# Kernel tuning notes

Measured on AMD Instinct MI355X. Metric: run time of the kernel, lower is better.

Reference implementation:

```python
import jax, jax.numpy as jnp
import numpy as np

B, N, U, D = 64, 1024, 128, 2   # batch, num_nodes, num_units, output_dim
K, L = 2, 2                     # max_diffusion_step, num_layers
NM = 2 * K + 1                  # num_matrices: 2 supports (dual random walk) * K + identity


def setup_inputs():
    key = jax.random.key(0)
    ks = jax.random.split(key, 16)
    d0, d1 = D + U, U + U       # gconv input_size per layer
    s = 0.05
    return {
        "inputs": jax.random.normal(ks[0], (B, N * D), jnp.float32),
        "hidden_state": jax.random.normal(ks[1], (L, B, N * U), jnp.float32),
        "adj": jax.random.uniform(ks[2], (N, N), dtype=jnp.float32),
        "gate_w0": jax.random.normal(ks[3], (d0 * NM, 2 * U), jnp.float32) * s,
        "gate_b0": jnp.ones((2 * U,), jnp.float32),   # bias_start=1.0 as in DCGRU gate
        "cand_w0": jax.random.normal(ks[4], (d0 * NM, U), jnp.float32) * s,
        "cand_b0": jnp.zeros((U,), jnp.float32),
        "gate_w1": jax.random.normal(ks[5], (d1 * NM, 2 * U), jnp.float32) * s,
        "gate_b1": jnp.ones((2 * U,), jnp.float32),
        "cand_w1": jax.random.normal(ks[6], (d1 * NM, U), jnp.float32) * s,
        "cand_b1": jnp.zeros((U,), jnp.float32),
        "proj_w": jax.random.normal(ks[7], (U, D), jnp.float32) * s,
        "proj_b": jnp.zeros((D,), jnp.float32),
    }


def _supports(adj):
    # dual random walk: [ (D_o^-1 A)^T, (D_i^-1 A^T)^T ]
    rw = lambda a: a / jnp.sum(a, axis=1, keepdims=True)
    return [rw(adj).T, rw(adj.T).T]


def _gconv(supports, x_bnd, h_bnd, w, b):
    # x_bnd: (B,N,in_dim), h_bnd: (B,N,U)
    in_size = x_bnd.shape[-1] + U
    x0 = jnp.transpose(jnp.concatenate([x_bnd, h_bnd], axis=-1), (1, 2, 0)).reshape(N, in_size * B)
    xs = [x0]
    for S in supports:
        xk_2, xk_1 = x0, S @ x0
        xs.append(xk_1)
        for _ in range(2, K + 1):
            xk = 2.0 * (S @ xk_1) - xk_2   # Chebyshev recursion
            xs.append(xk)
            xk_2, xk_1 = xk_1, xk
    x = jnp.stack(xs)                                   # (NM, N, in_size*B)
    x = x.reshape(NM, N, in_size, B).transpose(3, 1, 2, 0).reshape(B * N, in_size * NM)
    return x @ w + b                                    # (B*N, out)


def _dcgru_cell(supports, x_flat, h_flat, gw, gb, cw, cb, in_dim):
    xb = x_flat.reshape(B, N, in_dim)
    hb = h_flat.reshape(B, N, U)
    ru = jax.nn.sigmoid(_gconv(supports, xb, hb, gw, gb)).reshape(B, N, 2 * U)
    r, u = ru[..., :U], ru[..., U:]
    c = jnp.tanh(_gconv(supports, xb, r * hb, cw, cb)).reshape(B, N, U)
    return (u * hb + (1.0 - u) * c).reshape(B, N * U)


def reference(inputs, hidden_state, adj, gate_w0, gate_b0, cand_w0, cand_b0,
              gate_w1, gate_b1, cand_w1, cand_b1, proj_w, proj_b):
    sup = _supports(adj)
    h0 = _dcgru_cell(sup, inputs, hidden_state[0], gate_w0, gate_b0, cand_w0, cand_b0, D)
    h1 = _dcgru_cell(sup, h0, hidden_state[1], gate_w1, gate_b1, cand_w1, cand_b1, U)
    out = (h1.reshape(B * N, U) @ proj_w + proj_b).reshape(B, N * D)
    return out, jnp.stack([h0, h1])
```

## Files before the change

### kernel.cpp

```cpp
#include <hip/hip_runtime.h>
#include <hip/hip_bf16.h>

typedef unsigned short u16;
typedef unsigned int u32;
typedef __attribute__((ext_vector_type(2))) unsigned int u32x2;
typedef __attribute__((ext_vector_type(4))) float f32x4;
typedef __attribute__((ext_vector_type(8))) __bf16 bf16x8;

#define DEVI static __device__ __forceinline__

DEVI u16 f2bf(float x) {
  union { float f; u32 u; } v; v.f = x;
  u32 r = v.u + 0x7fffu + ((v.u >> 16) & 1u);
  return (u16)(r >> 16);
}
DEVI float bf2f(u16 h) { union { u32 u; float f; } v; v.u = ((u32)h) << 16; return v.f; }
DEVI u32 pk2bf(float a, float b) { return (u32)f2bf(a) | ((u32)f2bf(b) << 16); }
DEVI float sigm(float x) { return 1.f / (1.f + __expf(-x)); }
DEVI float tanh_(float x) {
  float a = fabsf(x);
  float e = __expf(-2.f * a);
  float t = (1.f - e) / (1.f + e);
  return copysignf(t, x);
}

DEVI void gl_lds16(const u16* g, void* l) {
  __builtin_amdgcn_global_load_lds(
      (const __attribute__((address_space(1))) u32*)(const void*)g,
      (__attribute__((address_space(3))) u32*)l, 16, 0, 0);
}
DEVI f32x4 mfma16(bf16x8 a, bf16x8 b, f32x4 c) {
  return __builtin_amdgcn_mfma_f32_16x16x32_bf16(a, b, c, 0, 0, 0);
}

#define SWZ(row) (((row) >> 1) & 3)

__global__ void sums_k(const float* __restrict__ adj, float* __restrict__ rs, float* __restrict__ cs) {
  __shared__ float red[256];
  int bid = blockIdx.x, tid = threadIdx.x;
  if (bid < 1024) {
    float a = 0.f;
    for (int j = tid; j < 1024; j += 256) a += adj[bid * 1024 + j];
    red[tid] = a; __syncthreads();
    for (int s = 128; s; s >>= 1) { if (tid < s) red[tid] += red[tid + s]; __syncthreads(); }
    if (!tid) rs[bid] = red[0];
  } else {
    int c0 = (bid - 1024) * 64;
    int c = tid & 63, r0 = tid >> 6;
    float a = 0.f;
    for (int r = r0; r < 1024; r += 4) a += adj[r * 1024 + c0 + c];
    red[tid] = a; __syncthreads();
    if (tid < 64) cs[c0 + c] = red[c] + red[64 + c] + red[128 + c] + red[192 + c];
  }
}

__global__ void s0_build(const float* __restrict__ adj, const float* __restrict__ rs, u16* __restrict__ S0) {
  __shared__ float tile[32][33];
  int i0 = blockIdx.x * 32, j0 = blockIdx.y * 32;
  int tx = threadIdx.x & 31, ty = threadIdx.x >> 5;
  for (int yy = ty; yy < 32; yy += 8)
    tile[yy][tx] = adj[(j0 + yy) * 1024 + i0 + tx];
  __syncthreads();
  for (int yy = ty; yy < 32; yy += 8)
    S0[(i0 + yy) * 1024 + j0 + tx] = f2bf(tile[tx][yy] / rs[j0 + tx]);
}

__global__ void s1_build(const float* __restrict__ adj, const float* __restrict__ cs, u16* __restrict__ S1) {
  int idx = blockIdx.x * 256 + threadIdx.x;
  int j = idx & 1023;
  S1[idx] = f2bf(adj[idx] / cs[j]);
}

__global__ void pack_w(const float* __restrict__ src, u16* __restrict__ dst,
                       int NO, int Ktot, int off0, int off1) {
  int idx = blockIdx.x * 256 + threadIdx.x;
  if (idx >= NO * Ktot) return;
  int o = idx / Ktot, k = idx % Ktot;
  int seg = k >> 7, i = k & 127;
  int mo = seg % 6;
  int pos = ((seg / 6) ? off1 : off0) + i;
  const float* wr = src + (long)pos * 5 * NO + o;
  float v;
  switch (mo) {
    case 0: case 1: v = wr[0] - wr[(long)2 * NO] - wr[(long)4 * NO]; break;
    case 2: v = wr[(long)1 * NO]; break;
    case 3: v = 2.f * wr[(long)2 * NO]; break;
    case 4: v = wr[(long)3 * NO]; break;
    default: v = 2.f * wr[(long)4 * NO]; break;
  }
  dst[idx] = f2bf(v);
}

__global__ void build_hx(const float* __restrict__ src, u16* __restrict__ hiN,
                         u16* __restrict__ loN, u16* __restrict__ hiT) {
  __shared__ u16 t[32][33];
  int n0 = blockIdx.x * 32, u0 = blockIdx.y * 32, b = blockIdx.z;
  int tx = threadIdx.x & 31, ty = threadIdx.x >> 5;
  for (int yy = ty; yy < 32; yy += 8) {
    long d = (long)b * 131072 + (n0 + yy) * 128 + u0 + tx;
    float v = src[d];
    u16 h = f2bf(v);
    hiN[d] = h;
    loN[d] = f2bf(v - bf2f(h));
    t[yy][tx] = h;
  }
  __syncthreads();
  for (int yy = ty; yy < 32; yy += 8)
    hiT[(long)(b * 128 + u0 + yy) * 1024 + n0 + tx] = t[tx][yy];
}

__global__ void xch0_build(const float* __restrict__ inp, float* __restrict__ x0) {
  int idx = blockIdx.x * 256 + threadIdx.x;
  int n = idx >> 7, c = idx & 127, b = c >> 1, d = c & 1;
  x0[idx] = inp[b * 2048 + n * 2 + d];
}

__global__ void xch_diffuse(const u16* __restrict__ S, const float* __restrict__ xin,
                            float* __restrict__ xout) {
  int n = blockIdx.x, c = threadIdx.x;
  float acc = 0.f;
  for (int k = 0; k < 1024; k++) acc += bf2f(S[n * 1024 + k]) * xin[k * 128 + c];
  xout[n * 128 + c] = acc;
}

__global__ void xch_cheb(const u16* __restrict__ S, const float* __restrict__ xin,
                         const float* __restrict__ x0, float* __restrict__ xout) {
  int n = blockIdx.x, c = threadIdx.x;
  float acc = 0.f;
  for (int k = 0; k < 1024; k++) acc += bf2f(S[n * 1024 + k]) * xin[k * 128 + c];
  xout[n * 128 + c] = 2.f * acc - x0[n * 128 + c];
}

__global__ void xg_build(const float* __restrict__ gw0, const float* __restrict__ cw0,
                         const float* __restrict__ xch,
                         u16* __restrict__ xgg, u16* __restrict__ xgc) {
  int r = blockIdx.x;
  int n = r & 1023, b = r >> 10;
  int t = threadIdx.x;
  __shared__ float xv[10];
  if (t < 10) { int m = t % 5, p = t / 5; xv[t] = xch[(long)m * 131072 + n * 128 + b * 2 + p]; }
  __syncthreads();
  float a = 0.f;
#pragma unroll
  for (int q = 0; q < 10; q++) { int m = q % 5, p = q / 5;
    a += gw0[(long)(p * 5 + m) * 256 + t] * xv[q]; }
  xgg[(long)r * 256 + t] = f2bf(a);
  if (t < 128) {
    float a2 = 0.f;
#pragma unroll
    for (int q = 0; q < 10; q++) { int m = q % 5, p = q / 5;
      a2 += cw0[(long)(p * 5 + m) * 128 + t] * xv[q]; }
    xgc[(long)r * 128 + t] = f2bf(a2);
  }
}

struct DiffJob { const u16* X; const u16* S; u16* YN; u16* YT; };
struct DiffJobs { DiffJob j[4]; };

__global__ __launch_bounds__(256, 2) void gemm_diffz(DiffJobs jobs) {
  DiffJob J = jobs.j[blockIdx.z];
  constexpr int ROWS = 384;
  constexpr int BUF = ROWS * 64;
  __shared__ char smem[3 * BUF];
  const int tid = threadIdx.x, wid = tid >> 6, lane = tid & 63;
  const int wrM = wid >> 1, wcN = wid & 1, l15 = lane & 15, l4 = lane >> 4;
  const int s_row = lane >> 2, s_kcp = lane & 3;
  const int ntile = blockIdx.y * 256;
  const int fbase = blockIdx.x * 128;

  f32x4 acc[8][4];
#pragma unroll
  for (int i = 0; i < 8; i++)
#pragma unroll
    for (int j = 0; j < 4; j++) acc[i][j] = (f32x4){0.f, 0.f, 0.f, 0.f};

  auto stage = [&](char* buf, int ks) {
    const int k0 = ks * 32;
#pragma unroll
    for (int c = 0; c < 6; c++) {
      const int row0 = c * 64 + wid * 16;
      const int row = row0 + s_row;
      const u16* src;
      if (row0 < 256) src = J.S + (long)(ntile + row) * 1024 + k0 + ((s_kcp ^ SWZ(row)) * 8);
      else { const int fr = row - 256; src = J.X + (long)(fbase + fr) * 1024 + k0 + ((s_kcp ^ SWZ(fr)) * 8); }
      gl_lds16(src, buf + row0 * 64);
    }
  };
  auto compute = [&](char* buf) {
    char* Ab = buf; char* Bb = buf + 256 * 64;
    bf16x8 af[8], bfr[4];
#pragma unroll
    for (int mb = 0; mb < 8; mb++) {
      const int row = wrM * 128 + mb * 16 + l15;
      af[mb] = *(const bf16x8*)(Ab + row * 64 + ((l4 ^ SWZ(row)) * 16));
    }
#pragma unroll
    for (int nb = 0; nb < 4; nb++) {
      const int row = wcN * 64 + nb * 16 + l15;
      bfr[nb] = *(const bf16x8*)(Bb + row * 64 + ((l4 ^ SWZ(row)) * 16));
    }
    __builtin_amdgcn_s_setprio(1);
#pragma unroll
    for (int mb = 0; mb < 8; mb++)
#pragma unroll
      for (int nb = 0; nb < 4; nb++)
        acc[mb][nb] = mfma16(af[mb], bfr[nb], acc[mb][nb]);
    __builtin_amdgcn_s_setprio(0);
  };

  const int NKS = 32;
  stage(smem, 0);
  stage(smem + BUF, 1);
  char* cur = smem; char* mid = smem + BUF; char* fut = smem + 2 * BUF;
  for (int ks = 0; ks + 2 < NKS; ks++) {
    stage(fut, ks + 2);
    asm volatile("s_waitcnt vmcnt(12)" ::: "memory");
    __builtin_amdgcn_s_barrier();
    __builtin_amdgcn_sched_barrier(0);
    compute(cur);
    asm volatile("" ::: "memory");
    __builtin_amdgcn_s_barrier();
    __builtin_amdgcn_sched_barrier(0);
    char* t = cur; cur = mid; mid = fut; fut = t;
  }
  asm volatile("s_waitcnt vmcnt(6)" ::: "memory");
  __builtin_amdgcn_s_barrier();
  __builtin_amdgcn_sched_barrier(0);
  compute(cur);
  asm volatile("s_waitcnt vmcnt(0)" ::: "memory");
  __builtin_amdgcn_s_barrier();
  __builtin_amdgcn_sched_barrier(0);
  compute(mid);

#pragma unroll
  for (int mb = 0; mb < 8; mb++) {
#pragma unroll
    for (int nb = 0; nb < 4; nb++) {
      const int n0 = ntile + wrM * 128 + mb * 16 + l4 * 4;
      const int f  = fbase + wcN * 64 + nb * 16 + l15;
      const int b = f >> 7, u = f & 127;
      f32x4 v = acc[mb][nb];
      u16 h0 = f2bf(v[0]), h1 = f2bf(v[1]), h2 = f2bf(v[2]), h3 = f2bf(v[3]);
      u16* yn = J.YN + (long)b * 131072 + (long)n0 * 128 + u;
      yn[0] = h0; yn[128] = h1; yn[256] = h2; yn[384] = h3;
      if (J.YT != nullptr) {
        u32x2 wv; wv[0] = (u32)h0 | ((u32)h1 << 16); wv[1] = (u32)h2 | ((u32)h3 << 16);
        *(u32x2*)(J.YT + (long)f * 1024 + n0) = wv;
      }
    }
  }
}

struct Segs { const u16* p[12]; };
DEVI const u16* seg_sel(const Segs& s, int i) {
  switch (i) {
    case 0: return s.p[0]; case 1: return s.p[1]; case 2: return s.p[2];
    case 3: return s.p[3]; case 4: return s.p[4]; case 5: return s.p[5];
    case 6: return s.p[6]; case 7: return s.p[7]; case 8: return s.p[8];
    case 9: return s.p[9]; case 10: return s.p[10]; default: return s.p[11];
  }
}

template<int EPI>
__global__ __launch_bounds__(256, 2) void gemm_wseg(
    Segs segs, const u16* __restrict__ WT, int Ktot,
    const float* __restrict__ bias, const float* __restrict__ Hprev,
    const u16* __restrict__ xadd,
    u16* __restrict__ rh_hi, u16* __restrict__ rh_lo, u16* __restrict__ rh_t,
    u16* __restrict__ usig,
    float* __restrict__ hnew_out, u16* __restrict__ xa_hi, u16* __restrict__ xa_lo,
    u16* __restrict__ xa_t)
{
  constexpr int TM = (EPI == 0) ? 256 : 128;
  constexpr int MB = (EPI == 0) ? 8 : 4;
  constexpr int MW = (EPI == 0) ? 128 : 64;
  constexpr int R1 = (TM + 128) / 64;
  constexpr int BUF = (TM + 128) * 64;
  __shared__ char smem[3 * BUF];
  const int tid = threadIdx.x, wid = tid >> 6, lane = tid & 63;
  const int wrM = wid >> 1, wcN = wid & 1, l15 = lane & 15, l4 = lane >> 4;
  const int s_row = lane >> 2, s_kcp = lane & 3;
  const int rtile = blockIdx.x * 128;

  f32x4 acc[MB][4];
#pragma unroll
  for (int i = 0; i < MB; i++)
#pragma unroll
    for (int j = 0; j < 4; j++) acc[i][j] = (f32x4){0.f, 0.f, 0.f, 0.f};

  const int NKS = Ktot >> 5;
  auto stage = [&](char* buf, int ks) {
    const int k0 = ks * 32;
    const int sidx = ks >> 2, si0 = (ks & 3) * 32;
    const u16* sp = seg_sel(segs, sidx);
#pragma unroll
    for (int c = 0; c < R1; c++) {
      const int row0 = c * 64 + wid * 16;
      const int row = row0 + s_row;
      const u16* src;
      if (row0 < TM) src = WT + (long)row * Ktot + k0 + ((s_kcp ^ SWZ(row)) * 8);
      else { const int br = row - TM; src = sp + (long)(rtile + br) * 128 + si0 + ((s_kcp ^ SWZ(br)) * 8); }
      gl_lds16(src, buf + row0 * 64);
    }
  };
  auto compute = [&](char* buf) {
    char* Ab = buf; char* Bb = buf + TM * 64;
    bf16x8 af[MB], bfr[4];
#pragma unroll
    for (int mb = 0; mb < MB; mb++) {
      const int row = wrM * MW + mb * 16 + l15;
      af[mb] = *(const bf16x8*)(Ab + row * 64 + ((l4 ^ SWZ(row)) * 16));
    }
#pragma unroll
    for (int nb = 0; nb < 4; nb++) {
      const int row = wcN * 64 + nb * 16 + l15;
      bfr[nb] = *(const bf16x8*)(Bb + row * 64 + ((l4 ^ SWZ(row)) * 16));
    }
    __builtin_amdgcn_s_setprio(1);
#pragma unroll
    for (int mb = 0; mb < MB; mb++)
#pragma unroll
      for (int nb = 0; nb < 4; nb++)
        acc[mb][nb] = mfma16(af[mb], bfr[nb], acc[mb][nb]);
    __builtin_amdgcn_s_setprio(0);
  };

  stage(smem, 0);
  stage(smem + BUF, 1);
  char* cur = smem; char* mid = smem + BUF; char* fut = smem + 2 * BUF;
  for (int ks = 0; ks + 2 < NKS; ks++) {
    stage(fut, ks + 2);
    if constexpr (R1 == 6) asm volatile("s_waitcnt vmcnt(12)" ::: "memory");
    else                   asm volatile("s_waitcnt vmcnt(8)" ::: "memory");
    __builtin_amdgcn_s_barrier();
    __builtin_amdgcn_sched_barrier(0);
    compute(cur);
    asm volatile("" ::: "memory");
    __builtin_amdgcn_s_barrier();
    __builtin_amdgcn_sched_barrier(0);
    char* t = cur; cur = mid; mid = fut; fut = t;
  }
  if constexpr (R1 == 6) asm volatile("s_waitcnt vmcnt(6)" ::: "memory");
  else                   asm volatile("s_waitcnt vmcnt(4)" ::: "memory");
  __builtin_amdgcn_s_barrier();
  __builtin_amdgcn_sched_barrier(0);
  compute(cur);
  asm volatile("s_waitcnt vmcnt(0)" ::: "memory");
  __builtin_amdgcn_s_barrier();
  __builtin_amdgcn_sched_barrier(0);
  compute(mid);

#pragma unroll
  for (int mb = 0; mb < MB; mb++) {
#pragma unroll
    for (int nb = 0; nb < 4; nb++) {
      const int o = wrM * MW + mb * 16 + l4 * 4;
      const int rr = rtile + wcN * 64 + nb * 16 + l15;
      const int n = rr & 1023, b = rr >> 10;
      f32x4 v = acc[mb][nb];
      float4 bv = *(const float4*)(bias + o);
      float a0 = 0.f, a1 = 0.f, a2 = 0.f, a3 = 0.f;
      if (xadd != nullptr) {
        const int xs = (EPI == 0) ? 256 : 128;
        u32x2 xv = *(const u32x2*)(xadd + (long)rr * xs + o);
        a0 = bf2f((u16)(xv[0] & 0xffffu)); a1 = bf2f((u16)(xv[0] >> 16));
        a2 = bf2f((u16)(xv[1] & 0xffffu)); a3 = bf2f((u16)(xv[1] >> 16));
      }
      if (EPI == 0) {
        float s0 = sigm(v[0] + bv.x + a0), s1 = sigm(v[1] + bv.y + a1);
        float s2 = sigm(v[2] + bv.z + a2), s3 = sigm(v[3] + bv.w + a3);
        if (o < 128) {
          float4 hv = *(const float4*)(Hprev + (long)rr * 128 + o);
          float r0 = s0 * hv.x, r1 = s1 * hv.y, r2 = s2 * hv.z, r3 = s3 * hv.w;
          u16 h0 = f2bf(r0), h1 = f2bf(r1), h2 = f2bf(r2), h3 = f2bf(r3);
          long d = (long)rr * 128 + o;
          u32x2 wh; wh[0] = (u32)h0 | ((u32)h1 << 16); wh[1] = (u32)h2 | ((u32)h3 << 16);
          *(u32x2*)(rh_hi + d) = wh;
          u32x2 wl; wl[0] = pk2bf(r0 - bf2f(h0), r1 - bf2f(h1));
          wl[1] = pk2bf(r2 - bf2f(h2), r3 - bf2f(h3));
          *(u32x2*)(rh_lo + d) = wl;
          u16* rt = rh_t + (long)(b * 128 + o) * 1024 + n;
          rt[0] = h0; rt[1024] = h1; rt[2048] = h2; rt[3072] = h3;
        } else {
          u32x2 wu; wu[0] = pk2bf(s0, s1); wu[1] = pk2bf(s2, s3);
          *(u32x2*)(usig + (long)rr * 128 + (o - 128)) = wu;
        }
      } else {
        float c0 = tanh_(v[0] + bv.x + a0), c1 = tanh_(v[1] + bv.y + a1);
        float c2 = tanh_(v[2] + bv.z + a2), c3 = tanh_(v[3] + bv.w + a3);
        u32x2 uv = *(const u32x2*)(usig + (long)rr * 128 + o);
        float u0 = bf2f((u16)(uv[0] & 0xffffu)), u1 = bf2f((u16)(uv[0] >> 16));
        float u2 = bf2f((u16)(uv[1] & 0xffffu)), u3 = bf2f((u16)(uv[1] >> 16));
        float4 hv = *(const float4*)(Hprev + (long)rr * 128 + o);
        float h0n = u0 * hv.x + (1.f - u0) * c0;
        float h1n = u1 * hv.y + (1.f - u1) * c1;
        float h2n = u2 * hv.z + (1.f - u2) * c2;
        float h3n = u3 * hv.w + (1.f - u3) * c3;
        *(float4*)(hnew_out + (long)rr * 128 + o) = make_float4(h0n, h1n, h2n, h3n);
        if (xa_hi != nullptr) {
          u16 x0 = f2bf(h0n), x1 = f2bf(h1n), x2 = f2bf(h2n), x3 = f2bf(h3n);
          long d = (long)rr * 128 + o;
          u32x2 wh; wh[0] = (u32)x0 | ((u32)x1 << 16); wh[1] = (u32)x2 | ((u32)x3 << 16);
          *(u32x2*)(xa_hi + d) = wh;
          u32x2 wl; wl[0] = pk2bf(h0n - bf2f(x0), h1n - bf2f(x1));
          wl[1] = pk2bf(h2n - bf2f(x2), h3n - bf2f(x3));
          *(u32x2*)(xa_lo + d) = wl;
          u16* xt = xa_t + (long)(b * 128 + o) * 1024 + n;
          xt[0] = x0; xt[1024] = x1; xt[2048] = x2; xt[3072] = x3;
        }
      }
    }
  }
}

__global__ __launch_bounds__(256) void proj_k(const float* __restrict__ h1n, const float* __restrict__ pw,
                                              const float* __restrict__ pb, float* __restrict__ out) {
  int wid = threadIdx.x >> 6, lane = threadIdx.x & 63;
  int r = blockIdx.x * 4 + wid;
  int b = r >> 10, n = r & 1023;
  const float* hp = h1n + (long)b * 131072 + n * 128;
  float ha = hp[lane], hb = hp[lane + 64];
  float p0 = ha * pw[lane * 2]     + hb * pw[(lane + 64) * 2];
  float p1 = ha * pw[lane * 2 + 1] + hb * pw[(lane + 64) * 2 + 1];
  for (int off = 32; off; off >>= 1) { p0 += __shfl_down(p0, off); p1 += __shfl_down(p1, off); }
  if (!lane) {
    out[(long)b * 2048 + n * 2]     = p0 + pb[0];
    out[(long)b * 2048 + n * 2 + 1] = p1 + pb[1];
  }
}

extern "C" void kernel_launch(void* const* d_in, const int* in_sizes, int n_in,
                              void* d_out, int out_size, void* d_ws, size_t ws_size,
                              hipStream_t stream) {
  (void)in_sizes; (void)n_in; (void)out_size; (void)ws_size;
  const float* inputs = (const float*)d_in[0];
  const float* hidden = (const float*)d_in[1];
  const float* adj    = (const float*)d_in[2];
  const float* gw0 = (const float*)d_in[3];
  const float* gb0 = (const float*)d_in[4];
  const float* cw0 = (const float*)d_in[5];
  const float* cb0 = (const float*)d_in[6];
  const float* gw1 = (const float*)d_in[7];
  const float* gb1 = (const float*)d_in[8];
  const float* cw1 = (const float*)d_in[9];
  const float* cb1 = (const float*)d_in[10];
  const float* pw  = (const float*)d_in[11];
  const float* pb  = (const float*)d_in[12];

  float* out    = (float*)d_out;
  float* out_h0 = out + 131072;
  float* out_h1 = out_h0 + 8388608;
  const float* h0 = hidden;
  const float* h1 = hidden + 8388608;

  u16* OH1a = (u16*)out_h1;
  u16* OH1b = OH1a + 8388608;

  char* wp = (char*)d_ws;
  auto alloc = [&](size_t bytes) { char* r = wp; wp += (bytes + 255) & ~(size_t)255; return r; };
  u16*   S0b  = (u16*)  alloc(1048576 * 2);
  u16*   S1b  = (u16*)  alloc(1048576 * 2);
  float* rs   = (float*)alloc(1024 * 4);
  float* cs   = (float*)alloc(1024 * 4);
  u16*   WG0  = (u16*)  alloc((size_t)256 * 768 * 2);
  u16*   WC0  = (u16*)  alloc((size_t)128 * 768 * 2);
  u16*   WG1  = (u16*)  alloc((size_t)256 * 1536 * 2);
  u16*   WC1  = (u16*)  alloc((size_t)128 * 1536 * 2);
  u16*   Bb   = (u16*)  alloc((size_t)13 * 8388608 * 2);
  u16*   USIG = (u16*)  alloc((size_t)8388608 * 2);
  float* XCH  = (float*)alloc((size_t)5 * 131072 * 4);
  auto BB = [&](int i) { return Bb + (size_t)i * 8388608; };
  auto XC = [&](int i) { return XCH + (size_t)i * 131072; };
  u16* XGg = BB(4);
  u16* XGc = BB(6);

  sums_k<<<1040, 256, 0, stream>>>(adj, rs, cs);
  s0_build<<<dim3(32, 32), 256, 0, stream>>>(adj, rs, S0b);
  s1_build<<<4096, 256, 0, stream>>>(adj, cs, S1b);
  pack_w<<<768,  256, 0, stream>>>(gw0, WG0, 256, 768, 2, 0);
  pack_w<<<384,  256, 0, stream>>>(cw0, WC0, 128, 768, 2, 0);
  pack_w<<<1536, 256, 0, stream>>>(gw1, WG1, 256, 1536, 0, 128);
  pack_w<<<768,  256, 0, stream>>>(cw1, WC1, 128, 1536, 0, 128);
  build_hx<<<dim3(32, 4, 64), 256, 0, stream>>>(h0, BB(0), BB(1), BB(2));
  build_hx<<<dim3(32, 4, 64), 256, 0, stream>>>(h1, OH1a, OH1b, BB(3));

  xch0_build<<<512, 256, 0, stream>>>(inputs, XC(0));
  xch_diffuse<<<1024, 128, 0, stream>>>(S0b, XC(0), XC(1));
  xch_cheb   <<<1024, 128, 0, stream>>>(S0b, XC(1), XC(0), XC(2));
  xch_diffuse<<<1024, 128, 0, stream>>>(S1b, XC(0), XC(3));
  xch_cheb   <<<1024, 128, 0, stream>>>(S1b, XC(3), XC(0), XC(4));
  xg_build<<<65536, 256, 0, stream>>>(gw0, cw0, XCH, XGg, XGc);

  DiffJobs dj{};
  dj.j[0] = {BB(2), S0b, BB(7), BB(8)};
  dj.j[1] = {BB(2), S1b, BB(9), BB(10)};
  gemm_diffz<<<dim3(64, 4, 2), 256, 0, stream>>>(dj);
  dj.j[0] = {BB(8),  S0b, BB(11), nullptr};
  dj.j[1] = {BB(10), S1b, BB(12), nullptr};
  gemm_diffz<<<dim3(64, 4, 2), 256, 0, stream>>>(dj);

  Segs sg0{};
  sg0.p[0] = BB(0); sg0.p[1] = BB(1); sg0.p[2] = BB(7); sg0.p[3] = BB(11); sg0.p[4] = BB(9); sg0.p[5] = BB(12);
  gemm_wseg<0><<<512, 256, 0, stream>>>(sg0, WG0, 768, gb0, h0, XGg,
      BB(2), BB(10), BB(8), USIG, nullptr, nullptr, nullptr, nullptr);

  dj.j[0] = {BB(8), S0b, BB(4), BB(5)};
  dj.j[1] = {BB(8), S1b, BB(0), BB(1)};
  gemm_diffz<<<dim3(64, 4, 2), 256, 0, stream>>>(dj);
  dj.j[0] = {BB(5), S0b, BB(7), nullptr};
  dj.j[1] = {BB(1), S1b, BB(9), nullptr};
  gemm_diffz<<<dim3(64, 4, 2), 256, 0, stream>>>(dj);

  Segs sc0{};
  sc0.p[0] = BB(2); sc0.p[1] = BB(10); sc0.p[2] = BB(4); sc0.p[3] = BB(7); sc0.p[4] = BB(0); sc0.p[5] = BB(9);
  gemm_wseg<1><<<512, 256, 0, stream>>>(sc0, WC0, 768, cb0, h0, XGc,
      nullptr, nullptr, nullptr, USIG, out_h0, BB(11), BB(12), BB(1));

  dj.j[0] = {BB(1), S0b, BB(0), BB(2)};
  dj.j[1] = {BB(1), S1b, BB(4), BB(5)};
  dj.j[2] = {BB(3), S0b, BB(8), BB(6)};
  dj.j[3] = {BB(3), S1b, BB(9), BB(7)};
  gemm_diffz<<<dim3(64, 4, 4), 256, 0, stream>>>(dj);
  dj.j[0] = {BB(2), S0b, BB(10), nullptr};
  dj.j[1] = {BB(5), S1b, BB(3),  nullptr};
  gemm_diffz<<<dim3(64, 4, 2), 256, 0, stream>>>(dj);
  dj.j[0] = {BB(6), S0b, BB(1), nullptr};
  dj.j[1] = {BB(7), S1b, BB(2), nullptr};
  gemm_diffz<<<dim3(64, 4, 2), 256, 0, stream>>>(dj);

  Segs sg1{};
  sg1.p[0] = BB(11); sg1.p[1] = BB(12); sg1.p[2] = BB(0); sg1.p[3] = BB(10); sg1.p[4] = BB(4); sg1.p[5] = BB(3);
  sg1.p[6] = OH1a;   sg1.p[7] = OH1b;   sg1.p[8] = BB(8); sg1.p[9] = BB(1);  sg1.p[10] = BB(9); sg1.p[11] = BB(2);
  gemm_wseg<0><<<512, 256, 0, stream>>>(sg1, WG1, 1536, gb1, h1, nullptr,
      BB(5), BB(7), BB(6), USIG, nullptr, nullptr, nullptr, nullptr);

  dj.j[0] = {BB(6), S0b, BB(8), BB(1)};
  dj.j[1] = {BB(6), S1b, BB(9), BB(2)};
  gemm_diffz<<<dim3(64, 4, 2), 256, 0, stream>>>(dj);
  dj.j[0] = {BB(1), S0b, BB(6), nullptr};
  gemm_diffz<<<dim3(64, 4, 1), 256, 0, stream>>>(dj);
  dj.j[0] = {BB(2), S1b, BB(1), nullptr};
  gemm_diffz<<<dim3(64, 4, 1), 256, 0, stream>>>(dj);

  Segs sc1{};
  sc1.p[0] = BB(11); sc1.p[1] = BB(12); sc1.p[2] = BB(0); sc1.p[3] = BB(10); sc1.p[4] = BB(4); sc1.p[5] = BB(3);
  sc1.p[6] = BB(5);  sc1.p[7] = BB(7);  sc1.p[8] = BB(8); sc1.p[9] = BB(6);  sc1.p[10] = BB(9); sc1.p[11] = BB(1);
  gemm_wseg<1><<<512, 256, 0, stream>>>(sc1, WC1, 1536, cb1, h1, nullptr,
      nullptr, nullptr, nullptr, USIG, out_h1, nullptr, nullptr, nullptr);

  proj_k<<<16384, 256, 0, stream>>>(out_h1, pw, pb, out);
}
```

Measured before the change: 1.115 ms.

## Drop bf16 hi/lo split of identity term and batch xg_build rows per block

Removes the low-residual bf16 copy of the hidden and intermediate states that the projection GEMMs used as an extra K-segment for the identity term. This shrinks the weight K from 6 to 5 segments per input and removes the lo writes in build_hx and both GEMM epilogues. Buffers are reassigned to match. Separately, xg_build now caches its weights in shared memory and processes 32 rows per block instead of one row per block. The cost is lower precision on the identity term of the graph convolution.

```diff
diff --git a/kernel.cpp b/kernel.cpp
--- a/kernel.cpp
+++ b/kernel.cpp
@@ -77,31 +77,29 @@
   if (idx >= NO * Ktot) return;
   int o = idx / Ktot, k = idx % Ktot;
   int seg = k >> 7, i = k & 127;
-  int mo = seg % 6;
-  int pos = ((seg / 6) ? off1 : off0) + i;
+  int mo = seg % 5;
+  int pos = ((seg / 5) ? off1 : off0) + i;
   const float* wr = src + (long)pos * 5 * NO + o;
   float v;
   switch (mo) {
-    case 0: case 1: v = wr[0] - wr[(long)2 * NO] - wr[(long)4 * NO]; break;
-    case 2: v = wr[(long)1 * NO]; break;
-    case 3: v = 2.f * wr[(long)2 * NO]; break;
-    case 4: v = wr[(long)3 * NO]; break;
+    case 0: v = wr[0] - wr[(long)2 * NO] - wr[(long)4 * NO]; break;
+    case 1: v = wr[(long)1 * NO]; break;
+    case 2: v = 2.f * wr[(long)2 * NO]; break;
+    case 3: v = wr[(long)3 * NO]; break;
     default: v = 2.f * wr[(long)4 * NO]; break;
   }
   dst[idx] = f2bf(v);
 }
 
 __global__ void build_hx(const float* __restrict__ src, u16* __restrict__ hiN,
-                         u16* __restrict__ loN, u16* __restrict__ hiT) {
+                         u16* __restrict__ hiT) {
   __shared__ u16 t[32][33];
   int n0 = blockIdx.x * 32, u0 = blockIdx.y * 32, b = blockIdx.z;
   int tx = threadIdx.x & 31, ty = threadIdx.x >> 5;
   for (int yy = ty; yy < 32; yy += 8) {
     long d = (long)b * 131072 + (n0 + yy) * 128 + u0 + tx;
-    float v = src[d];
-    u16 h = f2bf(v);
+    u16 h = f2bf(src[d]);
     hiN[d] = h;
-    loN[d] = f2bf(v - bf2f(h));
     t[yy][tx] = h;
   }
   __syncthreads();
@@ -131,26 +129,37 @@
   xout[n * 128 + c] = 2.f * acc - x0[n * 128 + c];
 }
 
-__global__ void xg_build(const float* __restrict__ gw0, const float* __restrict__ cw0,
-                         const float* __restrict__ xch,
-                         u16* __restrict__ xgg, u16* __restrict__ xgc) {
-  int r = blockIdx.x;
-  int n = r & 1023, b = r >> 10;
+__global__ __launch_bounds__(256) void xg_build(
+    const float* __restrict__ gw0, const float* __restrict__ cw0,
+    const float* __restrict__ xch,
+    u16* __restrict__ xgg, u16* __restrict__ xgc) {
+  __shared__ float wg[10][256];
+  __shared__ float wc[10][128];
+  __shared__ float xv[10];
   int t = threadIdx.x;
-  __shared__ float xv[10];
-  if (t < 10) { int m = t % 5, p = t / 5; xv[t] = xch[(long)m * 131072 + n * 128 + b * 2 + p]; }
+#pragma unroll
+  for (int q = 0; q < 10; q++) {
+    int m = q % 5, p = q / 5;
+    wg[q][t] = gw0[(long)(p * 5 + m) * 256 + t];
+    if (t < 128) wc[q][t] = cw0[(long)(p * 5 + m) * 128 + t];
+  }
   __syncthreads();
-  float a = 0.f;
-#pragma unroll
-  for (int q = 0; q < 10; q++) { int m = q % 5, p = q / 5;
-    a += gw0[(long)(p * 5 + m) * 256 + t] * xv[q]; }
-  xgg[(long)r * 256 + t] = f2bf(a);
-  if (t < 128) {
-    float a2 = 0.f;
-#pragma unroll
-    for (int q = 0; q < 10; q++) { int m = q % 5, p = q / 5;
-      a2 += cw0[(long)(p * 5 + m) * 128 + t] * xv[q]; }
-    xgc[(long)r * 128 + t] = f2bf(a2);
+  int r0 = blockIdx.x * 32;
+  for (int rl = 0; rl < 32; rl++) {
+    int r = r0 + rl, n = r & 1023, b = r >> 10;
+    if (t < 10) { int m = t % 5, p = t / 5; xv[t] = xch[(long)m * 131072 + n * 128 + b * 2 + p]; }
+    __syncthreads();
+    float a = 0.f;
+#pragma unroll
+    for (int q = 0; q < 10; q++) a += wg[q][t] * xv[q];
+    xgg[(long)r * 256 + t] = f2bf(a);
+    if (t < 128) {
+      float a2 = 0.f;
+#pragma unroll
+      for (int q = 0; q < 10; q++) a2 += wc[q][t] * xv[q];
+      xgc[(long)r * 128 + t] = f2bf(a2);
+    }
+    __syncthreads();
   }
 }
 
@@ -159,8 +168,7 @@
 
 __global__ __launch_bounds__(256, 2) void gemm_diffz(DiffJobs jobs) {
   DiffJob J = jobs.j[blockIdx.z];
-  constexpr int ROWS = 384;
-  constexpr int BUF = ROWS * 64;
+  constexpr int BUF = 384 * 64;
   __shared__ char smem[3 * BUF];
   const int tid = threadIdx.x, wid = tid >> 6, lane = tid & 63;
   const int wrM = wid >> 1, wcN = wid & 1, l15 = lane & 15, l4 = lane >> 4;
@@ -251,13 +259,13 @@
   }
 }
 
-struct Segs { const u16* p[12]; };
+struct Segs { const u16* p[10]; };
 DEVI const u16* seg_sel(const Segs& s, int i) {
   switch (i) {
     case 0: return s.p[0]; case 1: return s.p[1]; case 2: return s.p[2];
     case 3: return s.p[3]; case 4: return s.p[4]; case 5: return s.p[5];
     case 6: return s.p[6]; case 7: return s.p[7]; case 8: return s.p[8];
-    case 9: return s.p[9]; case 10: return s.p[10]; default: return s.p[11];
+    default: return s.p[9];
   }
 }
 
@@ -266,10 +274,8 @@
     Segs segs, const u16* __restrict__ WT, int Ktot,
     const float* __restrict__ bias, const float* __restrict__ Hprev,
     const u16* __restrict__ xadd,
-    u16* __restrict__ rh_hi, u16* __restrict__ rh_lo, u16* __restrict__ rh_t,
-    u16* __restrict__ usig,
-    float* __restrict__ hnew_out, u16* __restrict__ xa_hi, u16* __restrict__ xa_lo,
-    u16* __restrict__ xa_t)
+    u16* __restrict__ rh_hi, u16* __restrict__ rh_t, u16* __restrict__ usig,
+    float* __restrict__ hnew_out, u16* __restrict__ xa_hi, u16* __restrict__ xa_t)
 {
   constexpr int TM = (EPI == 0) ? 256 : 128;
   constexpr int MB = (EPI == 0) ? 8 : 4;
@@ -376,9 +382,6 @@
           long d = (long)rr * 128 + o;
           u32x2 wh; wh[0] = (u32)h0 | ((u32)h1 << 16); wh[1] = (u32)h2 | ((u32)h3 << 16);
           *(u32x2*)(rh_hi + d) = wh;
-          u32x2 wl; wl[0] = pk2bf(r0 - bf2f(h0), r1 - bf2f(h1));
-          wl[1] = pk2bf(r2 - bf2f(h2), r3 - bf2f(h3));
-          *(u32x2*)(rh_lo + d) = wl;
           u16* rt = rh_t + (long)(b * 128 + o) * 1024 + n;
           rt[0] = h0; rt[1024] = h1; rt[2048] = h2; rt[3072] = h3;
         } else {
@@ -402,9 +405,6 @@
           long d = (long)rr * 128 + o;
           u32x2 wh; wh[0] = (u32)x0 | ((u32)x1 << 16); wh[1] = (u32)x2 | ((u32)x3 << 16);
           *(u32x2*)(xa_hi + d) = wh;
-          u32x2 wl; wl[0] = pk2bf(h0n - bf2f(x0), h1n - bf2f(x1));
-          wl[1] = pk2bf(h2n - bf2f(x2), h3n - bf2f(x3));
-          *(u32x2*)(xa_lo + d) = wl;
           u16* xt = xa_t + (long)(b * 128 + o) * 1024 + n;
           xt[0] = x0; xt[1024] = x1; xt[2048] = x2; xt[3072] = x3;
         }
@@ -454,7 +454,6 @@
   const float* h1 = hidden + 8388608;
 
   u16* OH1a = (u16*)out_h1;
-  u16* OH1b = OH1a + 8388608;
 
   char* wp = (char*)d_ws;
   auto alloc = [&](size_t bytes) { char* r = wp; wp += (bytes + 255) & ~(size_t)255; return r; };
@@ -462,91 +461,90 @@
   u16*   S1b  = (u16*)  alloc(1048576 * 2);
   float* rs   = (float*)alloc(1024 * 4);
   float* cs   = (float*)alloc(1024 * 4);
-  u16*   WG0  = (u16*)  alloc((size_t)256 * 768 * 2);
-  u16*   WC0  = (u16*)  alloc((size_t)128 * 768 * 2);
-  u16*   WG1  = (u16*)  alloc((size_t)256 * 1536 * 2);
-  u16*   WC1  = (u16*)  alloc((size_t)128 * 1536 * 2);
+  u16*   WG0  = (u16*)  alloc((size_t)256 * 640 * 2);
+  u16*   WC0  = (u16*)  alloc((size_t)128 * 640 * 2);
+  u16*   WG1  = (u16*)  alloc((size_t)256 * 1280 * 2);
+  u16*   WC1  = (u16*)  alloc((size_t)128 * 1280 * 2);
   u16*   Bb   = (u16*)  alloc((size_t)13 * 8388608 * 2);
   u16*   USIG = (u16*)  alloc((size_t)8388608 * 2);
   float* XCH  = (float*)alloc((size_t)5 * 131072 * 4);
   auto BB = [&](int i) { return Bb + (size_t)i * 8388608; };
   auto XC = [&](int i) { return XCH + (size_t)i * 131072; };
-  u16* XGg = BB(4);
-  u16* XGc = BB(6);
+  u16* XGg = BB(3);
+  u16* XGc = BB(5);
 
   sums_k<<<1040, 256, 0, stream>>>(adj, rs, cs);
   s0_build<<<dim3(32, 32), 256, 0, stream>>>(adj, rs, S0b);
   s1_build<<<4096, 256, 0, stream>>>(adj, cs, S1b);
-  pack_w<<<768,  256, 0, stream>>>(gw0, WG0, 256, 768, 2, 0);
-  pack_w<<<384,  256, 0, stream>>>(cw0, WC0, 128, 768, 2, 0);
-  pack_w<<<1536, 256, 0, stream>>>(gw1, WG1, 256, 1536, 0, 128);
-  pack_w<<<768,  256, 0, stream>>>(cw1, WC1, 128, 1536, 0, 128);
-  build_hx<<<dim3(32, 4, 64), 256, 0, stream>>>(h0, BB(0), BB(1), BB(2));
-  build_hx<<<dim3(32, 4, 64), 256, 0, stream>>>(h1, OH1a, OH1b, BB(3));
+  pack_w<<<640,  256, 0, stream>>>(gw0, WG0, 256, 640, 2, 0);
+  pack_w<<<320,  256, 0, stream>>>(cw0, WC0, 128, 640, 2, 0);
+  pack_w<<<1280, 256, 0, stream>>>(gw1, WG1, 256, 1280, 0, 128);
+  pack_w<<<640,  256, 0, stream>>>(cw1, WC1, 128, 1280, 0, 128);
+  build_hx<<<dim3(32, 4, 64), 256, 0, stream>>>(h0, BB(0), BB(1));
+  build_hx<<<dim3(32, 4, 64), 256, 0, stream>>>(h1, OH1a, BB(2));
 
   xch0_build<<<512, 256, 0, stream>>>(inputs, XC(0));
   xch_diffuse<<<1024, 128, 0, stream>>>(S0b, XC(0), XC(1));
   xch_cheb   <<<1024, 128, 0, stream>>>(S0b, XC(1), XC(0), XC(2));
   xch_diffuse<<<1024, 128, 0, stream>>>(S1b, XC(0), XC(3));
   xch_cheb   <<<1024, 128, 0, stream>>>(S1b, XC(3), XC(0), XC(4));
-  xg_build<<<65536, 256, 0, stream>>>(gw0, cw0, XCH, XGg, XGc);
+  xg_build<<<2048, 256, 0, stream>>>(gw0, cw0, XCH, XGg, XGc);
 
   DiffJobs dj{};
-  dj.j[0] = {BB(2), S0b, BB(7), BB(8)};
-  dj.j[1] = {BB(2), S1b, BB(9), BB(10)};
-  gemm_diffz<<<dim3(64, 4, 2), 256, 0, stream>>>(dj);
-  dj.j[0] = {BB(8),  S0b, BB(11), nullptr};
-  dj.j[1] = {BB(10), S1b, BB(12), nullptr};
+  dj.j[0] = {BB(1), S0b, BB(6), BB(7)};
+  dj.j[1] = {BB(1), S1b, BB(8), BB(9)};
+  gemm_diffz<<<dim3(64, 4, 2), 256, 0, stream>>>(dj);
+  dj.j[0] = {BB(7), S0b, BB(10), nullptr};
+  dj.j[1] = {BB(9), S1b, BB(11), nullptr};
   gemm_diffz<<<dim3(64, 4, 2), 256, 0, stream>>>(dj);
 
   Segs sg0{};
-  sg0.p[0] = BB(0); sg0.p[1] = BB(1); sg0.p[2] = BB(7); sg0.p[3] = BB(11); sg0.p[4] = BB(9); sg0.p[5] = BB(12);
-  gemm_wseg<0><<<512, 256, 0, stream>>>(sg0, WG0, 768, gb0, h0, XGg,
-      BB(2), BB(10), BB(8), USIG, nullptr, nullptr, nullptr, nullptr);
-
-  dj.j[0] = {BB(8), S0b, BB(4), BB(5)};
-  dj.j[1] = {BB(8), S1b, BB(0), BB(1)};
-  gemm_diffz<<<dim3(64, 4, 2), 256, 0, stream>>>(dj);
-  dj.j[0] = {BB(5), S0b, BB(7), nullptr};
-  dj.j[1] = {BB(1), S1b, BB(9), nullptr};
+  sg0.p[0] = BB(0); sg0.p[1] = BB(6); sg0.p[2] = BB(10); sg0.p[3] = BB(8); sg0.p[4] = BB(11);
+  gemm_wseg<0><<<512, 256, 0, stream>>>(sg0, WG0, 640, gb0, h0, XGg,
+      BB(12), BB(1), USIG, nullptr, nullptr, nullptr);
+
+  dj.j[0] = {BB(1), S0b, BB(6), BB(7)};
+  dj.j[1] = {BB(1), S1b, BB(8), BB(9)};
+  gemm_diffz<<<dim3(64, 4, 2), 256, 0, stream>>>(dj);
+  dj.j[0] = {BB(7), S0b, BB(10), nullptr};
+  dj.j[1] = {BB(9), S1b, BB(11), nullptr};
   gemm_diffz<<<dim3(64, 4, 2), 256, 0, stream>>>(dj);
 
   Segs sc0{};
-  sc0.p[0] = BB(2); sc0.p[1] = BB(10); sc0.p[2] = BB(4); sc0.p[3] = BB(7); sc0.p[4] = BB(0); sc0.p[5] = BB(9);
-  gemm_wseg<1><<<512, 256, 0, stream>>>(sc0, WC0, 768, cb0, h0, XGc,
-      nullptr, nullptr, nullptr, USIG, out_h0, BB(11), BB(12), BB(1));
-
-  dj.j[0] = {BB(1), S0b, BB(0), BB(2)};
-  dj.j[1] = {BB(1), S1b, BB(4), BB(5)};
-  dj.j[2] = {BB(3), S0b, BB(8), BB(6)};
-  dj.j[3] = {BB(3), S1b, BB(9), BB(7)};
+  sc0.p[0] = BB(12); sc0.p[1] = BB(6); sc0.p[2] = BB(10); sc0.p[3] = BB(8); sc0.p[4] = BB(11);
+  gemm_wseg<1><<<512, 256, 0, stream>>>(sc0, WC0, 640, cb0, h0, XGc,
+      nullptr, nullptr, USIG, out_h0, BB(0), BB(1));
+
+  dj.j[0] = {BB(1), S0b, BB(3), BB(4)};
+  dj.j[1] = {BB(1), S1b, BB(5), BB(6)};
+  dj.j[2] = {BB(2), S0b, BB(7), BB(8)};
+  dj.j[3] = {BB(2), S1b, BB(9), BB(10)};
   gemm_diffz<<<dim3(64, 4, 4), 256, 0, stream>>>(dj);
-  dj.j[0] = {BB(2), S0b, BB(10), nullptr};
-  dj.j[1] = {BB(5), S1b, BB(3),  nullptr};
-  gemm_diffz<<<dim3(64, 4, 2), 256, 0, stream>>>(dj);
-  dj.j[0] = {BB(6), S0b, BB(1), nullptr};
-  dj.j[1] = {BB(7), S1b, BB(2), nullptr};
+  dj.j[0] = {BB(4), S0b, BB(11), nullptr};
+  dj.j[1] = {BB(6), S1b, BB(12), nullptr};
+  gemm_diffz<<<dim3(64, 4, 2), 256, 0, stream>>>(dj);
+  dj.j[0] = {BB(8), S0b, BB(4), nullptr};
+  dj.j[1] = {BB(10), S1b, BB(6), nullptr};
   gemm_diffz<<<dim3(64, 4, 2), 256, 0, stream>>>(dj);
 
   Segs sg1{};
-  sg1.p[0] = BB(11); sg1.p[1] = BB(12); sg1.p[2] = BB(0); sg1.p[3] = BB(10); sg1.p[4] = BB(4); sg1.p[5] = BB(3);
-  sg1.p[6] = OH1a;   sg1.p[7] = OH1b;   sg1.p[8] = BB(8); sg1.p[9] = BB(1);  sg1.p[10] = BB(9); sg1.p[11] = BB(2);
-  gemm_wseg<0><<<512, 256, 0, stream>>>(sg1, WG1, 1536, gb1, h1, nullptr,
-      BB(5), BB(7), BB(6), USIG, nullptr, nullptr, nullptr, nullptr);
-
-  dj.j[0] = {BB(6), S0b, BB(8), BB(1)};
-  dj.j[1] = {BB(6), S1b, BB(9), BB(2)};
-  gemm_diffz<<<dim3(64, 4, 2), 256, 0, stream>>>(dj);
-  dj.j[0] = {BB(1), S0b, BB(6), nullptr};
-  gemm_diffz<<<dim3(64, 4, 1), 256, 0, stream>>>(dj);
-  dj.j[0] = {BB(2), S1b, BB(1), nullptr};
-  gemm_diffz<<<dim3(64, 4, 1), 256, 0, stream>>>(dj);
+  sg1.p[0] = BB(0); sg1.p[1] = BB(3); sg1.p[2] = BB(11); sg1.p[3] = BB(5); sg1.p[4] = BB(12);
+  sg1.p[5] = OH1a;  sg1.p[6] = BB(7); sg1.p[7] = BB(4);  sg1.p[8] = BB(9); sg1.p[9] = BB(6);
+  gemm_wseg<0><<<512, 256, 0, stream>>>(sg1, WG1, 1280, gb1, h1, nullptr,
+      BB(8), BB(10), USIG, nullptr, nullptr, nullptr);
+
+  dj.j[0] = {BB(10), S0b, BB(1), BB(2)};
+  dj.j[1] = {BB(10), S1b, BB(7), BB(9)};
+  gemm_diffz<<<dim3(64, 4, 2), 256, 0, stream>>>(dj);
+  dj.j[0] = {BB(2), S0b, BB(4), nullptr};
+  dj.j[1] = {BB(9), S1b, BB(6), nullptr};
+  gemm_diffz<<<dim3(64, 4, 2), 256, 0, stream>>>(dj);
 
   Segs sc1{};
-  sc1.p[0] = BB(11); sc1.p[1] = BB(12); sc1.p[2] = BB(0); sc1.p[3] = BB(10); sc1.p[4] = BB(4); sc1.p[5] = BB(3);
-  sc1.p[6] = BB(5);  sc1.p[7] = BB(7);  sc1.p[8] = BB(8); sc1.p[9] = BB(6);  sc1.p[10] = BB(9); sc1.p[11] = BB(1);
-  gemm_wseg<1><<<512, 256, 0, stream>>>(sc1, WC1, 1536, cb1, h1, nullptr,
-      nullptr, nullptr, nullptr, USIG, out_h1, nullptr, nullptr, nullptr);
+  sc1.p[0] = BB(0); sc1.p[1] = BB(3); sc1.p[2] = BB(11); sc1.p[3] = BB(5); sc1.p[4] = BB(12);
+  sc1.p[5] = BB(8); sc1.p[6] = BB(1); sc1.p[7] = BB(4);  sc1.p[8] = BB(7); sc1.p[9] = BB(6);
+  gemm_wseg<1><<<512, 256, 0, stream>>>(sc1, WC1, 1280, cb1, h1, nullptr,
+      nullptr, nullptr, USIG, out_h1, nullptr, nullptr);
 
   proj_k<<<16384, 256, 0, stream>>>(out_h1, pw, pb, out);
 }
```

Measured after the change: 1.033 ms. -7.3%, faster.
